# Performance work log

Hardware: AMD Instinct MI355X
Metric: run time of the kernel (lower is better)

The kernel has to match this reference:

```python
import jax, jax.numpy as jnp
import numpy as np

N = 100_000          # nodes
E = 3_200_000        # edges (avg degree 32)
EMB = 16             # item embedding dim
IN = EMB + 1         # concat(embed, scalar feature)
HID = 32             # GAT hidden size
NEMB = 1000          # embedding vocab
SLOPE = 0.2          # GATConv leaky_relu negative slope


def setup_inputs() -> dict:
    key = jax.random.key(0)
    ks = jax.random.split(key, 24)
    g = lambda k, shape, fan: jax.random.normal(k, shape, dtype=jnp.float32) * (1.0 / np.sqrt(fan))
    inp = {
        "x_ids": jax.random.randint(ks[0], (N,), 0, NEMB, dtype=jnp.int32),
        "x_feat": jax.random.normal(ks[1], (N, 1), dtype=jnp.float32),
        "src": jax.random.randint(ks[2], (E,), 0, N, dtype=jnp.int32),
        "dst": jax.random.randint(ks[3], (E,), 0, N, dtype=jnp.int32),
        "edge_attr": jax.random.normal(ks[4], (E, 1), dtype=jnp.float32),
        # embedding table
        "emb": g(ks[5], (NEMB, EMB), EMB),
        # GATConv 1 (in=17, out=32, heads=1, edge_dim=1)
        "W1": g(ks[6], (IN, HID), IN),
        "a_s1": g(ks[7], (HID,), HID),
        "a_d1": g(ks[8], (HID,), HID),
        "We1": g(ks[9], (1, HID), 1),
        "a_e1": g(ks[10], (HID,), HID),
        "b1": jnp.zeros((HID,), jnp.float32),
        # GATConv 2 (in=32, out=32)
        "W2": g(ks[11], (HID, HID), HID),
        "a_s2": g(ks[12], (HID,), HID),
        "a_d2": g(ks[13], (HID,), HID),
        "We2": g(ks[14], (1, HID), 1),
        "a_e2": g(ks[15], (HID,), HID),
        "b2": jnp.zeros((HID,), jnp.float32),
        # final linear (32 -> 1)
        "lin_w": g(ks[16], (HID, 1), HID),
        "lin_b": jnp.zeros((1,), jnp.float32),
    }
    return inp


def _gat_conv(x, src, dst, eattr, W, a_s, a_d, We, a_e, b):
    """PyG GATConv (heads=1, concat=True) with edge features, self-loops already added."""
    h = x @ W                                   # [N, HID]
    alpha_src = h @ a_s                         # [N]
    alpha_dst = h @ a_d                         # [N]
    alpha_edge = (eattr @ We) @ a_e             # [E']
    alpha = jax.nn.leaky_relu(alpha_src[src] + alpha_dst[dst] + alpha_edge, SLOPE)
    # segment softmax over incoming edges of each dst node
    m = jax.ops.segment_max(alpha, dst, num_segments=N)
    ex = jnp.exp(alpha - m[dst])
    denom = jax.ops.segment_sum(ex, dst, num_segments=N)
    coef = ex / (denom[dst] + 1e-16)
    out = jax.ops.segment_sum(coef[:, None] * h[src], dst, num_segments=N)
    return out + b


def reference(x_ids, x_feat, src, dst, edge_attr, emb,
              W1, a_s1, a_d1, We1, a_e1, b1,
              W2, a_s2, a_d2, We2, a_e2, b2,
              lin_w, lin_b):
    # embedding lookup + concat scalar feature -> [N, 17]
    x = jnp.concatenate([emb[x_ids], x_feat], axis=1)

    # add self-loops once; self-loop edge_attr = mean of incoming edge attrs (fill_value='mean')
    loop = jnp.arange(N, dtype=src.dtype)
    deg = jax.ops.segment_sum(jnp.ones((E,), x.dtype), dst, num_segments=N)
    loop_attr = jax.ops.segment_sum(edge_attr, dst, num_segments=N) / jnp.maximum(deg, 1.0)[:, None]
    src2 = jnp.concatenate([src, loop])
    dst2 = jnp.concatenate([dst, loop])
    ea2 = jnp.concatenate([edge_attr, loop_attr], axis=0)

    x = _gat_conv(x, src2, dst2, ea2, W1, a_s1, a_d1, We1, a_e1, b1)
    x = jax.nn.relu(x)  # dropout is identity in eval mode
    x = _gat_conv(x, src2, dst2, ea2, W2, a_s2, a_d2, We2, a_e2, b2)
    return x @ lin_w + lin_b  # [N, 1]
```

## Files before the change

### kernel.cpp

```cpp
#include <hip/hip_runtime.h>

#define NN 100000
#define EE 3200000
#define SLOPE 0.2f

#define BKN 128
constexpr int NBK = (NN + BKN - 1) / BKN;
#define CAP 4544
constexpr int EP = EE + NN;

__global__ void k_bucket(const int* __restrict__ src, const int* __restrict__ dst,
                         const float* __restrict__ ea, int* __restrict__ cnt,
                         int2* __restrict__ stage) {
    __shared__ int hst[NBK];
    __shared__ int cur[NBK];
    int t = threadIdx.x;
    for (int i = t; i < NBK; i += 256) hst[i] = 0;
    __syncthreads();
    int base = blockIdx.x * 8192;
#pragma unroll 8
    for (int j = 0; j < 32; j++) {
        int e = base + j * 256 + t;
        if (e < EE) atomicAdd(&hst[dst[e] >> 7], 1);
    }
    __syncthreads();
    for (int i = t; i < NBK; i += 256)
        cur[i] = hst[i] ? atomicAdd(&cnt[i], hst[i]) : 0;
    __syncthreads();
    for (int j = 0; j < 32; j++) {
        int e = base + j * 256 + t;
        if (e < EE) {
            int d = dst[e];
            int bk = d >> 7;
            int pos = atomicAdd(&cur[bk], 1);
            if (pos < CAP)
                stage[(size_t)bk * CAP + pos] =
                    make_int2(src[e] | ((d & 127) << 17), __float_as_int(ea[e]));
        }
    }
}

__global__ void k_scanb(const int* __restrict__ cnt, int* __restrict__ fbase) {
    __shared__ int a[1024];
    int t = threadIdx.x;
    int v = 0;
    if (t < NBK) v = min(cnt[t], CAP) + min(BKN, NN - t * BKN);
    a[t] = v;
    __syncthreads();
    for (int off = 1; off < 1024; off <<= 1) {
        int x = (t >= off) ? a[t - off] : 0;
        __syncthreads();
        a[t] += x;
        __syncthreads();
    }
    if (t < NBK) fbase[t] = a[t] - v;
}

__global__ void k_build(const int* __restrict__ cnt, const int* __restrict__ fbase,
                        const int2* __restrict__ stage, int2* __restrict__ csr,
                        int* __restrict__ offs) {
    __shared__ int ldeg[BKN];
    __shared__ float esum[BKN];
    __shared__ int sc[BKN];
    __shared__ int lcur[BKN];
    int b = blockIdx.x, t = threadIdx.x;
    int nbase = b * BKN;
    int npb = min(BKN, NN - nbase);
    int c = min(cnt[b], CAP);
    const int2* ep = stage + (size_t)b * CAP;
    if (t < BKN) { ldeg[t] = 0; esum[t] = 0.f; }
    __syncthreads();
    for (int i = t; i < c; i += 256) {
        int2 e = ep[i];
        int n = (e.x >> 17) & 127;
        atomicAdd(&ldeg[n], 1);
        atomicAdd(&esum[n], __int_as_float(e.y));
    }
    __syncthreads();
    int v = (t < npb) ? ldeg[t] + 1 : 0;
    if (t < BKN) sc[t] = v;
    __syncthreads();
    for (int off = 1; off < BKN; off <<= 1) {
        int x = (t >= off && t < BKN) ? sc[t - off] : 0;
        __syncthreads();
        if (t < BKN) sc[t] += x;
        __syncthreads();
    }
    if (t < npb) {
        int start = fbase[b] + sc[t] - v;
        offs[nbase + t] = start;
        lcur[t] = start;
    }
    __syncthreads();
    for (int i = t; i < c; i += 256) {
        int2 e = ep[i];
        int n = (e.x >> 17) & 127;
        int pos = atomicAdd(&lcur[n], 1);
        csr[pos] = make_int2(e.x & 0x1FFFF, e.y);
    }
    __syncthreads();
    if (t < npb) {
        float mean = esum[t] / fmaxf((float)ldeg[t], 1.0f);
        csr[lcur[t]] = make_int2(nbase + t, __float_as_int(mean));
    }
    if (b == 0 && t == 0) offs[NN] = EP;
}

__global__ void k_const(const float* __restrict__ We1, const float* __restrict__ ae1,
                        const float* __restrict__ We2, const float* __restrict__ ae2,
                        float* __restrict__ cbuf) {
    int lane = threadIdx.x & 63;
    int comp = lane & 31;
    float p = (lane < 32) ? We1[comp] * ae1[comp] : We2[comp] * ae2[comp];
#pragma unroll
    for (int off = 16; off >= 1; off >>= 1) p += __shfl_xor(p, off);
    if (comp == 0) cbuf[lane >> 5] = p;
}


__global__ void k_h1(const int* __restrict__ ids, const float* __restrict__ feat,
                     const float* __restrict__ emb, const float* __restrict__ W,
                     const float* __restrict__ avs, const float* __restrict__ avd,
                     float* __restrict__ h, float* __restrict__ as_, float* __restrict__ ad_) {
    int n = blockIdx.x * 256 + threadIdx.x;
    if (n >= NN) return;
    float hv[32];
#pragma unroll
    for (int j = 0; j < 32; j++) hv[j] = 0.f;
    int id = ids[n];
    const float4* e4 = (const float4*)(emb + (size_t)id * 16);
#pragma unroll
    for (int k4 = 0; k4 < 4; k4++) {
        float4 xv = e4[k4];
        const float* wr = W + k4 * 4 * 32;
#pragma unroll
        for (int j = 0; j < 32; j++)
            hv[j] += xv.x * wr[j] + xv.y * wr[32 + j] + xv.z * wr[64 + j] + xv.w * wr[96 + j];
    }
    float f = feat[n];
#pragma unroll
    for (int j = 0; j < 32; j++) hv[j] += f * W[16 * 32 + j];
    float s = 0.f, d = 0.f;
#pragma unroll
    for (int j = 0; j < 32; j++) { s += hv[j] * avs[j]; d += hv[j] * avd[j]; }
    as_[n] = s;
    ad_[n] = d;
    float4* h4 = (float4*)(h + (size_t)n * 32);
#pragma unroll
    for (int q = 0; q < 8; q++)
        h4[q] = make_float4(hv[4 * q], hv[4 * q + 1], hv[4 * q + 2], hv[4 * q + 3]);
}

__global__ void k_h2(const float* __restrict__ x, const float* __restrict__ W,
                     const float* __restrict__ avs, const float* __restrict__ avd,
                     float* __restrict__ h, float* __restrict__ as_, float* __restrict__ ad_) {
    int n = blockIdx.x * 256 + threadIdx.x;
    if (n >= NN) return;
    float hv[32];
#pragma unroll
    for (int j = 0; j < 32; j++) hv[j] = 0.f;
    const float4* x4 = (const float4*)(x + (size_t)n * 32);
#pragma unroll
    for (int k4 = 0; k4 < 8; k4++) {
        float4 xv = x4[k4];
        const float* wr = W + k4 * 4 * 32;
#pragma unroll
        for (int j = 0; j < 32; j++)
            hv[j] += xv.x * wr[j] + xv.y * wr[32 + j] + xv.z * wr[64 + j] + xv.w * wr[96 + j];
    }
    float s = 0.f, d = 0.f;
#pragma unroll
    for (int j = 0; j < 32; j++) { s += hv[j] * avs[j]; d += hv[j] * avd[j]; }
    as_[n] = s;
    ad_[n] = d;
    float4* h4 = (float4*)(h + (size_t)n * 32);
#pragma unroll
    for (int q = 0; q < 8; q++)
        h4[q] = make_float4(hv[4 * q], hv[4 * q + 1], hv[4 * q + 2], hv[4 * q + 3]);
}

template <bool FINAL>
__global__ void k_gat(const int* __restrict__ offs, const int2* __restrict__ csr,
                      const float* __restrict__ h, const float* __restrict__ as_,
                      const float* __restrict__ ad_, const float* __restrict__ cbuf,
                      int cidx, const float* __restrict__ bias,
                      const float* __restrict__ lw, const float* __restrict__ lb,
                      float* __restrict__ out) {
    __shared__ int2 xb[4][64];
    int wid = threadIdx.x >> 6;
    int node = blockIdx.x * 4 + wid;
    if (node >= NN) return;
    int lane = threadIdx.x & 63;
    int comp = lane & 31;
    int slot = lane >> 5;
    int base = offs[node];
    int cnt = offs[node + 1] - base;
    float c = cbuf[cidx];
    float adn = ad_[node];
    float acc0 = 0.f, acc1 = 0.f, acc2 = 0.f, acc3 = 0.f, exs = 0.f;
    for (int cb = 0; cb < cnt; cb += 64) {
        int idx = cb + lane;
        bool val = idx < cnt;
        int2 e = csr[base + (val ? idx : 0)];
        int s = e.x;
        float a = as_[s] + adn + c * __int_as_float(e.y);
        a = (a >= 0.f) ? a : SLOPE * a;
        float ex = val ? __expf(a) : 0.f;
        exs += ex;
        xb[wid][lane] = make_int2(s << 5, __float_as_int(ex));
        int m = min(cnt - cb, 64);
        for (int j = 0; j < m; j += 8) {
            int2 p0 = xb[wid][j + slot];
            int2 p1 = xb[wid][j + 2 + slot];
            int2 p2 = xb[wid][j + 4 + slot];
            int2 p3 = xb[wid][j + 6 + slot];
            acc0 += __int_as_float(p0.y) * h[p0.x + comp];
            acc1 += __int_as_float(p1.y) * h[p1.x + comp];
            acc2 += __int_as_float(p2.y) * h[p2.x + comp];
            acc3 += __int_as_float(p3.y) * h[p3.x + comp];
        }
    }
    float acc = (acc0 + acc1) + (acc2 + acc3);
    acc += __shfl_xor(acc, 32);
#pragma unroll
    for (int off = 1; off < 64; off <<= 1) exs += __shfl_xor(exs, off);
    float o = acc / (exs + 1e-16f) + bias[comp];
    if (!FINAL) {
        o = fmaxf(o, 0.f);
        if (lane < 32) out[(size_t)node * 32 + comp] = o;
    } else {
        float y = o * lw[comp];
#pragma unroll
        for (int off = 16; off >= 1; off >>= 1) y += __shfl_xor(y, off);
        if (lane == 0) out[node] = y + lb[0];
    }
}


extern "C" void kernel_launch(void* const* d_in, const int* in_sizes, int n_in,
                              void* d_out, int out_size, void* d_ws, size_t ws_size,
                              hipStream_t stream) {
    const int* x_ids = (const int*)d_in[0];
    const float* x_feat = (const float*)d_in[1];
    const int* src = (const int*)d_in[2];
    const int* dst = (const int*)d_in[3];
    const float* eattr = (const float*)d_in[4];
    const float* emb = (const float*)d_in[5];
    const float* W1 = (const float*)d_in[6];
    const float* a_s1 = (const float*)d_in[7];
    const float* a_d1 = (const float*)d_in[8];
    const float* We1 = (const float*)d_in[9];
    const float* a_e1 = (const float*)d_in[10];
    const float* b1 = (const float*)d_in[11];
    const float* W2 = (const float*)d_in[12];
    const float* a_s2 = (const float*)d_in[13];
    const float* a_d2 = (const float*)d_in[14];
    const float* We2 = (const float*)d_in[15];
    const float* a_e2 = (const float*)d_in[16];
    const float* b2 = (const float*)d_in[17];
    const float* lin_w = (const float*)d_in[18];
    const float* lin_b = (const float*)d_in[19];

    char* p = (char*)d_ws;
    auto alloc = [&](size_t bytes) {
        void* r = (void*)p;
        p += (bytes + 255) & ~(size_t)255;
        return r;
    };
    int* cnt = (int*)alloc(NBK * 4);
    int* fbase = (int*)alloc(NBK * 4);
    float* cbuf = (float*)alloc(2 * 4);
    int* offs = (int*)alloc((NN + 1) * 4);
    float* asb = (float*)alloc(NN * 4);
    float* adb = (float*)alloc(NN * 4);
    int2* csr = (int2*)alloc((size_t)EP * 8);
    void* regionA = alloc((size_t)NBK * CAP * 8);
    int2* stage = (int2*)regionA;
    float* hbuf = (float*)regionA;
    float* x2 = hbuf + (size_t)NN * 32;
    (void)ws_size; (void)in_sizes; (void)n_in; (void)out_size;

    hipMemsetAsync(cnt, 0, NBK * 4, stream);

    const int BB = (EE + 8191) / 8192;
    const int NBT = (NN + 255) / 256;
    const int NW = (NN + 3) / 4;

    k_bucket<<<BB, 256, 0, stream>>>(src, dst, eattr, cnt, stage);
    k_scanb<<<1, 1024, 0, stream>>>(cnt, fbase);
    k_build<<<NBK, 256, 0, stream>>>(cnt, fbase, stage, csr, offs);
    k_const<<<1, 64, 0, stream>>>(We1, a_e1, We2, a_e2, cbuf);

    k_h1<<<NBT, 256, 0, stream>>>(x_ids, x_feat, emb, W1, a_s1, a_d1, hbuf, asb, adb);
    k_gat<false><<<NW, 256, 0, stream>>>(offs, csr, hbuf, asb, adb, cbuf, 0, b1,
                                         nullptr, nullptr, x2);
    k_h2<<<NBT, 256, 0, stream>>>(x2, W2, a_s2, a_d2, hbuf, asb, adb);
    k_gat<true><<<NW, 256, 0, stream>>>(offs, csr, hbuf, asb, adb, cbuf, 1, b2,
                                        lin_w, lin_b, (float*)d_out);
}
```

Before: 379.0 us.

## Sort edges by bucket in shared memory before coalesced scatter to stage

The bucketing kernel now processes 4096 edges per block, keeping each edge's src, dst and attribute in registers so they are read only once. It computes a block-local prefix scan over the bucket histogram and places records contiguously by bucket in shared memory. The records are then written to global memory in sorted order, so writes to the same bucket land in consecutive addresses instead of scattered 8-byte stores. The cost is about 53 KB of shared memory per block, lower occupancy, and an extra in-block scan with several barriers.

After: 352.5 us. 7.0% less time.

```diff
diff --git a/kernel.cpp b/kernel.cpp
--- a/kernel.cpp
+++ b/kernel.cpp
@@ -8,35 +8,74 @@
 constexpr int NBK = (NN + BKN - 1) / BKN;
 #define CAP 4544
 constexpr int EP = EE + NN;
+#define EPB 4096
+constexpr int NBB = (EE + EPB - 1) / EPB;
 
 __global__ void k_bucket(const int* __restrict__ src, const int* __restrict__ dst,
                          const float* __restrict__ ea, int* __restrict__ cnt,
                          int2* __restrict__ stage) {
     __shared__ int hst[NBK];
-    __shared__ int cur[NBK];
+    __shared__ int scl[NBK];
+    __shared__ int gdel[NBK];
+    __shared__ int aux[256];
+    __shared__ int2 rec[EPB];
+    __shared__ int addr[EPB];
     int t = threadIdx.x;
+    int base = blockIdx.x * EPB;
+    int nedge = min(EPB, EE - base);
     for (int i = t; i < NBK; i += 256) hst[i] = 0;
     __syncthreads();
-    int base = blockIdx.x * 8192;
-#pragma unroll 8
-    for (int j = 0; j < 32; j++) {
+    int ds[16], ss[16]; float es[16];
+#pragma unroll
+    for (int j = 0; j < 16; j++) {
         int e = base + j * 256 + t;
-        if (e < EE) atomicAdd(&hst[dst[e] >> 7], 1);
-    }
-    __syncthreads();
-    for (int i = t; i < NBK; i += 256)
-        cur[i] = hst[i] ? atomicAdd(&cnt[i], hst[i]) : 0;
-    __syncthreads();
-    for (int j = 0; j < 32; j++) {
-        int e = base + j * 256 + t;
-        if (e < EE) {
-            int d = dst[e];
-            int bk = d >> 7;
-            int pos = atomicAdd(&cur[bk], 1);
-            if (pos < CAP)
-                stage[(size_t)bk * CAP + pos] =
-                    make_int2(src[e] | ((d & 127) << 17), __float_as_int(ea[e]));
+        bool v = e < EE;
+        ds[j] = v ? dst[e] : -1;
+        ss[j] = v ? src[e] : 0;
+        es[j] = v ? ea[e] : 0.f;
+        if (v) atomicAdd(&hst[ds[j] >> 7], 1);
+    }
+    __syncthreads();
+    int i0 = t * 4;
+    int v0 = (i0 + 0 < NBK) ? hst[i0 + 0] : 0;
+    int v1 = (i0 + 1 < NBK) ? hst[i0 + 1] : 0;
+    int v2 = (i0 + 2 < NBK) ? hst[i0 + 2] : 0;
+    int v3 = (i0 + 3 < NBK) ? hst[i0 + 3] : 0;
+    int tsum = v0 + v1 + v2 + v3;
+    aux[t] = tsum;
+    __syncthreads();
+    for (int off = 1; off < 256; off <<= 1) {
+        int x = (t >= off) ? aux[t - off] : 0;
+        __syncthreads();
+        aux[t] += x;
+        __syncthreads();
+    }
+    int ex = aux[t] - tsum;
+    if (i0 + 0 < NBK) scl[i0 + 0] = ex;
+    if (i0 + 1 < NBK) scl[i0 + 1] = ex + v0;
+    if (i0 + 2 < NBK) scl[i0 + 2] = ex + v0 + v1;
+    if (i0 + 3 < NBK) scl[i0 + 3] = ex + v0 + v1 + v2;
+    __syncthreads();
+    for (int i = t; i < NBK; i += 256) {
+        int h = hst[i];
+        int g = h ? atomicAdd(&cnt[i], h) : 0;
+        gdel[i] = (g + i * CAP) - scl[i];
+    }
+    __syncthreads();
+#pragma unroll
+    for (int j = 0; j < 16; j++) {
+        if (ds[j] >= 0) {
+            int bk = ds[j] >> 7;
+            int pos = atomicAdd(&scl[bk], 1);
+            int gpos = pos + gdel[bk];
+            rec[pos] = make_int2(ss[j] | ((ds[j] & 127) << 17), __float_as_int(es[j]));
+            addr[pos] = (gpos - bk * CAP < CAP) ? gpos : -1;
         }
+    }
+    __syncthreads();
+    for (int i = t; i < nedge; i += 256) {
+        int a = addr[i];
+        if (a >= 0) stage[a] = rec[i];
     }
 }
 
@@ -282,11 +321,10 @@
 
     hipMemsetAsync(cnt, 0, NBK * 4, stream);
 
-    const int BB = (EE + 8191) / 8192;
     const int NBT = (NN + 255) / 256;
     const int NW = (NN + 3) / 4;
 
-    k_bucket<<<BB, 256, 0, stream>>>(src, dst, eattr, cnt, stage);
+    k_bucket<<<NBB, 256, 0, stream>>>(src, dst, eattr, cnt, stage);
     k_scanb<<<1, 1024, 0, stream>>>(cnt, fbase);
     k_build<<<NBK, 256, 0, stream>>>(cnt, fbase, stage, csr, offs);
     k_const<<<1, 64, 0, stream>>>(We1, a_e1, We2, a_e2, cbuf);
```
